# Performance work log

Hardware: AMD Instinct MI355X
Metric: run time of the kernel (lower is better)

The kernel has to match this reference:

```python
import jax, jax.numpy as jnp
import numpy as np

# NF4 codebook (bitsandbytes / torchao canonical 16 levels)
_NF4 = np.array([
    -1.0, -0.6961928009986877, -0.5250730514526367, -0.39491748809814453,
    -0.28444138169288635, -0.18477343022823334, -0.09105003625154495, 0.0,
    0.07958029955625534, 0.16093020141124725, 0.24611230194568634,
    0.33791524171829224, 0.44070982933044434, 0.5626170039176941,
    0.7229568362236023, 1.0], dtype=np.float32)

IN_DIM = 4096
OUT_DIM = 4096
RANK = 16
ALPHA = 32.0
BLOCK = 64  # NF4 quantization block size along in_dim


def setup_inputs() -> dict:
    key = jax.random.key(0)
    k1, k2, k3, k4, k5 = jax.random.split(key, 5)
    x = jax.random.normal(k1, (4, 2048, IN_DIM), dtype=jnp.float32)
    # 4-bit codes for the frozen base weight [out_dim, in_dim]
    w_q = jax.random.randint(k2, (OUT_DIM, IN_DIM), 0, 16, dtype=jnp.int32)
    # per-block absmax scales: [out_dim, in_dim // BLOCK]
    scales = jax.random.uniform(k3, (OUT_DIM, IN_DIM // BLOCK), dtype=jnp.float32)
    lora_a_w = jax.random.normal(k4, (RANK, IN_DIM), dtype=jnp.float32) * (1.0 / np.sqrt(IN_DIM))
    lora_b_w = jax.random.normal(k5, (OUT_DIM, RANK), dtype=jnp.float32) * 0.02
    return {"x": x, "w_q": w_q, "scales": scales,
            "lora_a_w": lora_a_w, "lora_b_w": lora_b_w}


def _dequant_nf4(w_q, scales):
    # w_q: [out, in] int codes; scales: [out, in//BLOCK]
    codebook = jnp.asarray(_NF4)
    w = codebook[w_q]  # [out, in]
    w = w.reshape(w.shape[0], -1, BLOCK) * scales[:, :, None]
    return w.reshape(w_q.shape)  # [out, in]


def reference(x, w_q, scales, lora_a_w, lora_b_w):
    # base path: dequantized NF4 linear (frozen, no bias)
    w = _dequant_nf4(w_q, scales)          # [out, in]
    out = jnp.einsum('bsi,oi->bso', x, w)  # [B, S, out]
    # LoRA path: dropout is Identity (p=0.0)
    a = jnp.einsum('bsi,ri->bsr', x, lora_a_w)      # [B, S, r]
    lora_out = jnp.einsum('bsr,or->bso', a, lora_b_w)  # [B, S, out]
    return out + (ALPHA / RANK) * lora_out
```

## Files before the change

kernel.cpp:

```cpp
#include <hip/hip_runtime.h>

typedef unsigned int u32;
typedef unsigned short u16;
typedef __bf16 bf16x8 __attribute__((ext_vector_type(8)));
typedef float f32x4 __attribute__((ext_vector_type(4)));

#define M_TOT 8192
#define N_TOT 4096
#define K_TOT 4096
#define RANK 16

__constant__ float NF4_TAB[16] = {
    -1.0f, -0.6961928009986877f, -0.5250730514526367f, -0.39491748809814453f,
    -0.28444138169288635f, -0.18477343022823334f, -0.09105003625154495f, 0.0f,
    0.07958029955625534f, 0.16093020141124725f, 0.24611230194568634f,
    0.33791524171829224f, 0.44070982933044434f, 0.5626170039176941f,
    0.7229568362236023f, 1.0f};

__device__ __forceinline__ u16 f2bf(float f) {
  u32 u = __builtin_bit_cast(u32, f);
  return (u16)((u + 0x7FFFu + ((u >> 16) & 1u)) >> 16);
}

__device__ __forceinline__ void async_copy16(const u16* g, u16* l) {
  __builtin_amdgcn_global_load_lds(
      (const __attribute__((address_space(1))) u32*)g,
      (__attribute__((address_space(3))) u32*)l, 16, 0, 0);
}

__global__ __launch_bounds__(256) void cvt_kernel(const float* __restrict__ x,
                                                  u16* __restrict__ xb) {
  int t = blockIdx.x * 256 + threadIdx.x;
  const float4* xv = (const float4*)x;
  float4 v0 = xv[2 * t], v1 = xv[2 * t + 1];
  uint4 o;
  o.x = (u32)f2bf(v0.x) | ((u32)f2bf(v0.y) << 16);
  o.y = (u32)f2bf(v0.z) | ((u32)f2bf(v0.w) << 16);
  o.z = (u32)f2bf(v1.x) | ((u32)f2bf(v1.y) << 16);
  o.w = (u32)f2bf(v1.z) | ((u32)f2bf(v1.w) << 16);
  ((uint4*)xb)[t] = o;
}

__global__ __launch_bounds__(256) void dequant_kernel(
    const int* __restrict__ wq, const float* __restrict__ scales,
    const float* __restrict__ Aw, const float* __restrict__ Bw,
    u16* __restrict__ Wb) {
  __shared__ float Bs[16 * RANK];
  int t = threadIdx.x;
  int o0 = blockIdx.y * 16;
  int tabi = __builtin_bit_cast(int, NF4_TAB[t & 15]);
  Bs[t] = Bw[o0 * RANK + t];
  __syncthreads();

  int i0 = blockIdx.x * 1024 + t * 4;
  float a[RANK][4];
#pragma unroll
  for (int r = 0; r < RANK; ++r) {
    float4 v = *(const float4*)(Aw + r * K_TOT + i0);
    a[r][0] = v.x; a[r][1] = v.y; a[r][2] = v.z; a[r][3] = v.w;
  }
#pragma unroll
  for (int j = 0; j < 16; ++j) {
    int o = o0 + j;
    int4 q = *(const int4*)(wq + (size_t)o * K_TOT + i0);
    float s = scales[o * (K_TOT / 64) + (i0 >> 6)];
    float d0 = 0.f, d1 = 0.f, d2 = 0.f, d3 = 0.f;
#pragma unroll
    for (int r = 0; r < RANK; ++r) {
      float b = Bs[j * RANK + r];
      d0 += b * a[r][0]; d1 += b * a[r][1];
      d2 += b * a[r][2]; d3 += b * a[r][3];
    }
    float t0 = __builtin_bit_cast(float, __builtin_amdgcn_ds_bpermute((q.x & 15) << 2, tabi));
    float t1 = __builtin_bit_cast(float, __builtin_amdgcn_ds_bpermute((q.y & 15) << 2, tabi));
    float t2 = __builtin_bit_cast(float, __builtin_amdgcn_ds_bpermute((q.z & 15) << 2, tabi));
    float t3 = __builtin_bit_cast(float, __builtin_amdgcn_ds_bpermute((q.w & 15) << 2, tabi));
    float w0 = t0 * s + 2.0f * d0;
    float w1 = t1 * s + 2.0f * d1;
    float w2 = t2 * s + 2.0f * d2;
    float w3 = t3 * s + 2.0f * d3;
    uint2 ov;
    ov.x = (u32)f2bf(w0) | ((u32)f2bf(w1) << 16);
    ov.y = (u32)f2bf(w2) | ((u32)f2bf(w3) << 16);
    *(uint2*)(Wb + (size_t)o * K_TOT + i0) = ov;
  }
}

__global__ __launch_bounds__(256) void gemm_kernel(const u16* __restrict__ A,
                                                   const u16* __restrict__ B,
                                                   float* __restrict__ C) {
  __shared__ __align__(16) u16 As[128 * 64];
  __shared__ __align__(16) u16 Bs[128 * 64];

  int tid = threadIdx.x;
  int bn = blockIdx.x, bm = blockIdx.y;
  int lane = tid & 63, wave = tid >> 6;
  int wm = wave & 1, wn = wave >> 1;

  int srow = lane >> 3;
  int sg = (lane & 7) ^ srow;
  const u16 *gA[4], *gB[4];
  u16 *lA[4], *lB[4];
#pragma unroll
  for (int t = 0; t < 4; ++t) {
    int rb = (wave * 4 + t) * 8;
    gA[t] = A + (size_t)(bm * 128 + rb + srow) * K_TOT + sg * 8;
    gB[t] = B + (size_t)(bn * 128 + rb + srow) * K_TOT + sg * 8;
    lA[t] = As + rb * 64 + lane * 8;
    lB[t] = Bs + rb * 64 + lane * 8;
  }

  int m = lane & 15, q = lane >> 4;
  int x7 = m & 7;
  const u16* pA = As + (wm * 64 + m) * 64;
  const u16* pB = Bs + (wn * 64 + m) * 64;
  int off0 = (q ^ x7) << 3;
  int off1 = ((q + 4) ^ x7) << 3;

  f32x4 acc[4][4] = {};

  for (int k0 = 0; k0 < K_TOT; k0 += 64) {
#pragma unroll
    for (int t = 0; t < 4; ++t) {
      async_copy16(gA[t] + k0, lA[t]);
      async_copy16(gB[t] + k0, lB[t]);
    }
    __syncthreads();

#pragma unroll
    for (int kk = 0; kk < 2; ++kk) {
      int off = kk ? off1 : off0;
      bf16x8 af[4], bfr[4];
#pragma unroll
      for (int i = 0; i < 4; ++i) {
        af[i] = *(const bf16x8*)(pA + i * 16 * 64 + off);
        bfr[i] = *(const bf16x8*)(pB + i * 16 * 64 + off);
      }
#pragma unroll
      for (int i = 0; i < 4; ++i)
#pragma unroll
        for (int j = 0; j < 4; ++j)
          acc[i][j] = __builtin_amdgcn_mfma_f32_16x16x32_bf16(af[i], bfr[j],
                                                              acc[i][j], 0, 0, 0);
    }
    __syncthreads();
  }

  int r0 = bm * 128 + wm * 64 + (q << 2);
  int c0 = bn * 128 + wn * 64 + m;
#pragma unroll
  for (int i = 0; i < 4; ++i)
#pragma unroll
    for (int j = 0; j < 4; ++j)
#pragma unroll
      for (int p = 0; p < 4; ++p)
        C[(size_t)(r0 + i * 16 + p) * N_TOT + (c0 + j * 16)] = acc[i][j][p];
}

extern "C" void kernel_launch(void* const* d_in, const int* in_sizes, int n_in,
                              void* d_out, int out_size, void* d_ws, size_t ws_size,
                              hipStream_t stream) {
  const float* x = (const float*)d_in[0];
  const int* wq = (const int*)d_in[1];
  const float* scales = (const float*)d_in[2];
  const float* Aw = (const float*)d_in[3];
  const float* Bw = (const float*)d_in[4];
  float* out = (float*)d_out;

  u16* xb = (u16*)d_ws;
  u16* Wb = (u16*)((char*)d_ws + (size_t)M_TOT * K_TOT * 2);

  cvt_kernel<<<(M_TOT * K_TOT) / (256 * 8), 256, 0, stream>>>(x, xb);
  dequant_kernel<<<dim3(K_TOT / 1024, N_TOT / 16), 256, 0, stream>>>(wq, scales, Aw, Bw, Wb);
  gemm_kernel<<<dim3(N_TOT / 128, M_TOT / 128), 256, 0, stream>>>(xb, Wb, out);
}
```

Measured before the change: 601.8 us.

## Rewrite GEMM with 256x256 tiles, double-buffered LDS and interleaved MFMA phases

Replaces the 128x128 single-buffer GEMM with a 256x256 tile, 512-thread kernel that double-buffers LDS. Global-to-LDS copies for the next K step are issued between MFMA phases, and each phase is fenced by s_barrier and raised priority. Block IDs are swizzled so neighbouring blocks share tiles in L2. The aim is to hide load latency and raise reuse per LDS byte, at the cost of 128KB of LDS per block and higher register pressure.

```diff
diff --git a/kernel.cpp b/kernel.cpp
--- a/kernel.cpp
+++ b/kernel.cpp
@@ -9,6 +9,11 @@
 #define N_TOT 4096
 #define K_TOT 4096
 #define RANK 16
+
+#define BM 256
+#define BN 256
+#define BK 64
+#define NT (K_TOT / BK)
 
 __constant__ float NF4_TAB[16] = {
     -1.0f, -0.6961928009986877f, -0.5250730514526367f, -0.39491748809814453f,
@@ -86,70 +91,127 @@
   }
 }
 
-__global__ __launch_bounds__(256) void gemm_kernel(const u16* __restrict__ A,
-                                                   const u16* __restrict__ B,
-                                                   float* __restrict__ C) {
-  __shared__ __align__(16) u16 As[128 * 64];
-  __shared__ __align__(16) u16 Bs[128 * 64];
+#define STAGE_A(buf, k0, i) \
+  async_copy16(gA + (size_t)(i) * 64 * K_TOT + (k0), &sh[buf][0][(i) * 4096 + tid * 8])
+#define STAGE_B(buf, k0, i) \
+  async_copy16(gB + (size_t)(i) * 64 * K_TOT + (k0), &sh[buf][1][(i) * 4096 + tid * 8])
+
+#define LOAD_A(mh)                                              \
+  do {                                                          \
+    const u16* p_ = sA + (wm * 128 + (mh) * 64 + m) * 64;       \
+    _Pragma("unroll") for (int i_ = 0; i_ < 4; ++i_) {          \
+      af[i_][0] = *(const bf16x8*)(p_ + i_ * 16 * 64 + off0);   \
+      af[i_][1] = *(const bf16x8*)(p_ + i_ * 16 * 64 + off1);   \
+    }                                                           \
+  } while (0)
+
+#define LOAD_B(nh)                                              \
+  do {                                                          \
+    const u16* p_ = sB + (wn * 64 + (nh) * 32 + m) * 64;        \
+    _Pragma("unroll") for (int j_ = 0; j_ < 2; ++j_) {          \
+      bfr[j_][0] = *(const bf16x8*)(p_ + j_ * 16 * 64 + off0);  \
+      bfr[j_][1] = *(const bf16x8*)(p_ + j_ * 16 * 64 + off1);  \
+    }                                                           \
+  } while (0)
+
+#define PHASE_TAIL(mh, nh)                                                  \
+  do {                                                                      \
+    __builtin_amdgcn_s_barrier();                                           \
+    asm volatile("s_waitcnt lgkmcnt(0)" ::: "memory");                      \
+    __builtin_amdgcn_sched_barrier(0);                                      \
+    __builtin_amdgcn_s_setprio(1);                                          \
+    _Pragma("unroll") for (int kk_ = 0; kk_ < 2; ++kk_)                     \
+    _Pragma("unroll") for (int i_ = 0; i_ < 4; ++i_)                        \
+    _Pragma("unroll") for (int j_ = 0; j_ < 2; ++j_)                        \
+      acc[(mh) * 4 + i_][(nh) * 2 + j_] =                                   \
+          __builtin_amdgcn_mfma_f32_16x16x32_bf16(                          \
+              af[i_][kk_], bfr[j_][kk_], acc[(mh) * 4 + i_][(nh) * 2 + j_], \
+              0, 0, 0);                                                     \
+    __builtin_amdgcn_s_setprio(0);                                          \
+    __builtin_amdgcn_s_barrier();                                           \
+  } while (0)
+
+__global__ __launch_bounds__(512, 2) void gemm_kernel(const u16* __restrict__ A,
+                                                      const u16* __restrict__ B,
+                                                      float* __restrict__ C) {
+  __shared__ __align__(16) u16 sh[2][2][BM * BK];
 
   int tid = threadIdx.x;
-  int bn = blockIdx.x, bm = blockIdx.y;
   int lane = tid & 63, wave = tid >> 6;
-  int wm = wave & 1, wn = wave >> 1;
-
-  int srow = lane >> 3;
-  int sg = (lane & 7) ^ srow;
-  const u16 *gA[4], *gB[4];
-  u16 *lA[4], *lB[4];
-#pragma unroll
-  for (int t = 0; t < 4; ++t) {
-    int rb = (wave * 4 + t) * 8;
-    gA[t] = A + (size_t)(bm * 128 + rb + srow) * K_TOT + sg * 8;
-    gB[t] = B + (size_t)(bn * 128 + rb + srow) * K_TOT + sg * 8;
-    lA[t] = As + rb * 64 + lane * 8;
-    lB[t] = Bs + rb * 64 + lane * 8;
-  }
+  int wm = wave >> 2, wn = wave & 3;
+
+  int bid = blockIdx.y * gridDim.x + blockIdx.x;
+  int swz = (bid & 7) * 64 + (bid >> 3);
+  int bm = swz >> 4, bn = swz & 15;
+
+  int srow = tid >> 3;
+  int sg = (tid & 7) ^ (srow & 7);
+  const u16* gA = A + (size_t)(bm * BM + srow) * K_TOT + sg * 8;
+  const u16* gB = B + (size_t)(bn * BN + srow) * K_TOT + sg * 8;
 
   int m = lane & 15, q = lane >> 4;
   int x7 = m & 7;
-  const u16* pA = As + (wm * 64 + m) * 64;
-  const u16* pB = Bs + (wn * 64 + m) * 64;
   int off0 = (q ^ x7) << 3;
   int off1 = ((q + 4) ^ x7) << 3;
 
-  f32x4 acc[4][4] = {};
-
-  for (int k0 = 0; k0 < K_TOT; k0 += 64) {
-#pragma unroll
-    for (int t = 0; t < 4; ++t) {
-      async_copy16(gA[t] + k0, lA[t]);
-      async_copy16(gB[t] + k0, lB[t]);
-    }
-    __syncthreads();
-
-#pragma unroll
-    for (int kk = 0; kk < 2; ++kk) {
-      int off = kk ? off1 : off0;
-      bf16x8 af[4], bfr[4];
-#pragma unroll
-      for (int i = 0; i < 4; ++i) {
-        af[i] = *(const bf16x8*)(pA + i * 16 * 64 + off);
-        bfr[i] = *(const bf16x8*)(pB + i * 16 * 64 + off);
-      }
-#pragma unroll
-      for (int i = 0; i < 4; ++i)
-#pragma unroll
-        for (int j = 0; j < 4; ++j)
-          acc[i][j] = __builtin_amdgcn_mfma_f32_16x16x32_bf16(af[i], bfr[j],
-                                                              acc[i][j], 0, 0, 0);
-    }
-    __syncthreads();
-  }
-
-  int r0 = bm * 128 + wm * 64 + (q << 2);
-  int c0 = bn * 128 + wn * 64 + m;
-#pragma unroll
-  for (int i = 0; i < 4; ++i)
+  f32x4 acc[8][4] = {};
+  bf16x8 af[4][2], bfr[2][2];
+
+#pragma unroll
+  for (int i = 0; i < 4; ++i) {
+    STAGE_A(0, 0, i);
+    STAGE_B(0, 0, i);
+  }
+
+  for (int t = 0; t < NT - 1; ++t) {
+    int cur = t & 1, nxt = cur ^ 1;
+    int k1 = (t + 1) * BK;
+    const u16* sA = sh[cur][0];
+    const u16* sB = sh[cur][1];
+
+#pragma unroll
+    for (int i = 0; i < 4; ++i) STAGE_A(nxt, k1, i);
+    asm volatile("s_waitcnt vmcnt(4)" ::: "memory");
+    __builtin_amdgcn_s_barrier();
+
+    LOAD_A(0);
+    LOAD_B(0);
+    STAGE_B(nxt, k1, 0);
+    STAGE_B(nxt, k1, 1);
+    PHASE_TAIL(0, 0);
+
+    LOAD_B(1);
+    STAGE_B(nxt, k1, 2);
+    STAGE_B(nxt, k1, 3);
+    PHASE_TAIL(0, 1);
+
+    LOAD_A(1);
+    PHASE_TAIL(1, 1);
+
+    LOAD_B(0);
+    PHASE_TAIL(1, 0);
+  }
+
+  {
+    const u16* sA = sh[(NT - 1) & 1][0];
+    const u16* sB = sh[(NT - 1) & 1][1];
+    asm volatile("s_waitcnt vmcnt(0)" ::: "memory");
+    __builtin_amdgcn_s_barrier();
+    LOAD_A(0);
+    LOAD_B(0);
+    PHASE_TAIL(0, 0);
+    LOAD_B(1);
+    PHASE_TAIL(0, 1);
+    LOAD_A(1);
+    PHASE_TAIL(1, 1);
+    LOAD_B(0);
+    PHASE_TAIL(1, 0);
+  }
+
+  int r0 = bm * BM + wm * 128 + (q << 2);
+  int c0 = bn * BN + wn * 64 + m;
+#pragma unroll
+  for (int i = 0; i < 8; ++i)
 #pragma unroll
     for (int j = 0; j < 4; ++j)
 #pragma unroll
@@ -172,5 +234,5 @@
 
   cvt_kernel<<<(M_TOT * K_TOT) / (256 * 8), 256, 0, stream>>>(x, xb);
   dequant_kernel<<<dim3(K_TOT / 1024, N_TOT / 16), 256, 0, stream>>>(wq, scales, Aw, Bw, Wb);
-  gemm_kernel<<<dim3(N_TOT / 128, M_TOT / 128), 256, 0, stream>>>(xb, Wb, out);
-}
+  gemm_kernel<<<dim3(N_TOT / BN, M_TOT / BM), 512, 0, stream>>>(xb, Wb, out);
+}
```

Measured after the change: 514.5 us. 14.5% less time.
